# Optimization experiments

Measured on AMD Instinct MI355X. Metric: run time of the kernel, lower is better.

## Reference

```python
import jax, jax.numpy as jnp
import numpy as np
from jax import lax

N_LAYERS, N_HIDDEN, IN_DIM, WARMUP, T_STEPS = 3, 1024, 256, 64, 2048


def setup_inputs() -> dict:
    key = jax.random.key(0)
    ks = jax.random.split(key, 16)
    s = 0.03  # keep gate pre-activations sane
    return {
        "x": jax.random.uniform(ks[0], (1, IN_DIM, WARMUP), jnp.float32),
        "h0": jax.random.normal(ks[1], (N_LAYERS, N_HIDDEN), jnp.float32),
        "c0": jax.random.normal(ks[2], (N_LAYERS, N_HIDDEN), jnp.float32),
        "W_ih0": jax.random.normal(ks[3], (4 * N_HIDDEN, IN_DIM), jnp.float32) * s,
        "W_hh0": jax.random.normal(ks[4], (4 * N_HIDDEN, N_HIDDEN), jnp.float32) * s,
        "W_ih1": jax.random.normal(ks[5], (4 * N_HIDDEN, N_HIDDEN), jnp.float32) * s,
        "W_hh1": jax.random.normal(ks[6], (4 * N_HIDDEN, N_HIDDEN), jnp.float32) * s,
        "W_ih2": jax.random.normal(ks[7], (4 * N_HIDDEN, N_HIDDEN), jnp.float32) * s,
        "W_hh2": jax.random.normal(ks[8], (4 * N_HIDDEN, N_HIDDEN), jnp.float32) * s,
        "b_ih": jax.random.normal(ks[9], (N_LAYERS, 4 * N_HIDDEN), jnp.float32) * s,
        "b_hh": jax.random.normal(ks[10], (N_LAYERS, 4 * N_HIDDEN), jnp.float32) * s,
        "W_fc": jax.random.normal(ks[11], (IN_DIM, N_HIDDEN), jnp.float32) * s,
        "b_fc": jax.random.normal(ks[12], (IN_DIM,), jnp.float32) * s,
        "timesteps": T_STEPS,
    }


def _lstm_cell(inp, h, c, W_ih, W_hh, bi, bh):
    # PyTorch gate order: i, f, g, o
    g = W_ih @ inp + W_hh @ h + bi + bh  # (4H,)
    i, f, gg, o = jnp.split(g, 4)
    c_new = jax.nn.sigmoid(f) * c + jax.nn.sigmoid(i) * jnp.tanh(gg)
    h_new = jax.nn.sigmoid(o) * jnp.tanh(c_new)
    return h_new, c_new


def reference(x, h0, c0, W_ih0, W_hh0, W_ih1, W_hh1, W_ih2, W_hh2, b_ih, b_hh, W_fc, b_fc, timesteps):
    T = int(timesteps)
    L = x.shape[2]
    D = x.shape[1]
    x_seq = x[0].T  # (L, D) teacher-forcing inputs (batch must be 1, per original reshape)
    x_pad = jnp.zeros((T, D), x.dtype).at[:L].set(x_seq)

    def step(carry, s):
        h, c, prev = carry  # h, c: (3, H)
        h = lax.stop_gradient(h)  # hn.detach()
        c = lax.stop_gradient(c)  # cn.detach()
        inp = jnp.where(s < L, x_pad[s], prev)
        h0n, c0n = _lstm_cell(inp, h[0], c[0], W_ih0, W_hh0, b_ih[0], b_hh[0])
        h1n, c1n = _lstm_cell(h0n, h[1], c[1], W_ih1, W_hh1, b_ih[1], b_hh[1])
        h2n, c2n = _lstm_cell(h1n, h[2], c[2], W_ih2, W_hh2, b_ih[2], b_hh[2])
        gen = jax.nn.sigmoid(W_fc @ lax.stop_gradient(h2n) + b_fc)  # fc on detached lstm out
        nxt = jnp.where(s + 1 < L, x_pad[s + 1], gen)
        new_carry = (jnp.stack([h0n, h1n, h2n]), jnp.stack([c0n, c1n, c2n]), nxt)
        return new_carry, nxt

    init = (h0, c0, x_seq[0])
    _, outs = lax.scan(step, init, jnp.arange(T - 1))  # (T-1, D)
    out = jnp.concatenate([x_seq[0:1], outs], axis=0)  # (T, D)
    return out.T[None]  # (1, D, T)
```

## Files before the change

### kernel.cpp

```cpp
#include <hip/hip_runtime.h>
#include <math.h>

#define H 1024
#define D 256
#define NB 256
#define NT 512
#define LW 64
#define STRIDE 32

typedef float f32x4 __attribute__((ext_vector_type(4)));

__device__ __forceinline__ float sigf(float v) { return 1.f / (1.f + __expf(-v)); }

__device__ __forceinline__ float waveReduce(float v) {
#pragma unroll
    for (int off = 32; off > 0; off >>= 1) v += __shfl_xor(v, off, 64);
    return v;
}

__device__ __forceinline__ f32x4 ldg4_nw(const float* p) {
    f32x4 r;
    asm volatile("global_load_dwordx4 %0, %1, off sc0 sc1" : "=v"(r) : "v"(p) : "memory");
    return r;
}
__device__ __forceinline__ float ldg1_nw(const float* p) {
    float r;
    asm volatile("global_load_dword %0, %1, off sc0 sc1" : "=v"(r) : "v"(p) : "memory");
    return r;
}
__device__ __forceinline__ void vm_wait4(f32x4& a, f32x4& b, f32x4& c, f32x4& d) {
    asm volatile("s_waitcnt vmcnt(0)" : "+v"(a), "+v"(b), "+v"(c), "+v"(d) :: "memory");
    __builtin_amdgcn_sched_barrier(0);
}
__device__ __forceinline__ void vm_wait4f(float& a, float& b, float& c, float& d) {
    asm volatile("s_waitcnt vmcnt(0)" : "+v"(a), "+v"(b), "+v"(c), "+v"(d) :: "memory");
    __builtin_amdgcn_sched_barrier(0);
}
__device__ __forceinline__ void stg4_sc(float* p, f32x4 v) {
    asm volatile("global_store_dwordx4 %0, %1, off sc0 sc1" :: "v"(p), "v"(v) : "memory");
}
__device__ __forceinline__ void stg1_sc(float* p, float v) {
    asm volatile("global_store_dword %0, %1, off sc0 sc1" :: "v"(p), "v"(v) : "memory");
}

__device__ __forceinline__ float tagf(int i) { return 8.0f * (float)(i & 3) - 12.0f; }
__device__ __forceinline__ bool vld4(f32x4 c, float tg) {
    float m = fmaxf(fmaxf(fabsf(c.x - tg), fabsf(c.y - tg)),
                    fmaxf(fabsf(c.z - tg), fabsf(c.w - tg)));
    return m < 2.0f;
}

#define EXN ((1 + 6) * NB * STRIDE)
__device__ float g_ex[EXN];

__global__ void ws_clear() {
    int i = blockIdx.x * blockDim.x + threadIdx.x;
    for (; i < EXN; i += gridDim.x * blockDim.x) g_ex[i] = 0.f;
}

__global__ __launch_bounds__(NT, 2) void rnn_reg8(
    const float* __restrict__ x, const float* __restrict__ h0in, const float* __restrict__ c0,
    const float* __restrict__ Wih0, const float* __restrict__ Whh0,
    const float* __restrict__ Wih1, const float* __restrict__ Whh1,
    const float* __restrict__ Wih2, const float* __restrict__ Whh2,
    const float* __restrict__ b_ih, const float* __restrict__ b_hh,
    const float* __restrict__ Wfc, const float* __restrict__ bfc,
    float* __restrict__ out, int T, int L)
{
    const int b = blockIdx.x;
    const int tid = threadIdx.x;
    const int w = tid >> 6;
    const int lane = tid & 63;
    const int gate = w & 3;
    const int up = w >> 2;
    const int u0 = b * 4 + 2 * up;
    const int r0 = gate * H + u0;
    const int r1 = r0 + 1;
    const int off = lane * 4;

    float* inpw = g_ex;

    __shared__ __align__(16) float lds_h0[2 * H], lds_h1[2 * H], lds_h2[2 * H];
    __shared__ __align__(16) float lds_fc[H];
    __shared__ __align__(16) float lds_inp[D];
    __shared__ float lds_x[LW];
    __shared__ float gate_buf[16];
    __shared__ float red[8];
    __shared__ float c_st[12];

    float4 wA0[5], wB0[5], wA1[8], wB1[8], wA2[8], wB2[8];
    wA0[0] = *(const float4*)(Wih0 + (size_t)r0 * 256 + off);
    wB0[0] = *(const float4*)(Wih0 + (size_t)r1 * 256 + off);
#pragma unroll
    for (int j = 0; j < 4; ++j) {
        wA0[j + 1] = *(const float4*)(Whh0 + (size_t)r0 * H + j * 256 + off);
        wB0[j + 1] = *(const float4*)(Whh0 + (size_t)r1 * H + j * 256 + off);
        wA1[j]     = *(const float4*)(Wih1 + (size_t)r0 * H + j * 256 + off);
        wB1[j]     = *(const float4*)(Wih1 + (size_t)r1 * H + j * 256 + off);
        wA1[j + 4] = *(const float4*)(Whh1 + (size_t)r0 * H + j * 256 + off);
        wB1[j + 4] = *(const float4*)(Whh1 + (size_t)r1 * H + j * 256 + off);
        wA2[j]     = *(const float4*)(Wih2 + (size_t)r0 * H + j * 256 + off);
        wB2[j]     = *(const float4*)(Wih2 + (size_t)r1 * H + j * 256 + off);
        wA2[j + 4] = *(const float4*)(Whh2 + (size_t)r0 * H + j * 256 + off);
        wB2[j + 4] = *(const float4*)(Whh2 + (size_t)r1 * H + j * 256 + off);
    }
    const float bA0 = b_ih[r0] + b_hh[r0];
    const float bB0 = b_ih[r1] + b_hh[r1];
    const float bA1 = b_ih[4 * H + r0] + b_hh[4 * H + r0];
    const float bB1 = b_ih[4 * H + r1] + b_hh[4 * H + r1];
    const float bA2 = b_ih[8 * H + r0] + b_hh[8 * H + r0];
    const float bB2 = b_ih[8 * H + r1] + b_hh[8 * H + r1];
    const float bfc_b = bfc[b];

#define KA(v) asm volatile("" : "+v"(v.x), "+v"(v.y), "+v"(v.z), "+v"(v.w))
#pragma unroll
    for (int j = 0; j < 5; ++j) { KA(wA0[j]); KA(wB0[j]); }
#pragma unroll
    for (int j = 0; j < 8; ++j) { KA(wA1[j]); KA(wB1[j]); KA(wA2[j]); KA(wB2[j]); }
#undef KA

    for (int i = tid; i < H; i += NT) {
        lds_fc[i]     = Wfc[(size_t)b * H + i];
        lds_h0[H + i] = h0in[i];
        lds_h1[H + i] = h0in[H + i];
        lds_h2[H + i] = h0in[2 * H + i];
    }
    if (tid < LW && tid < L) lds_x[tid] = x[(size_t)b * L + tid];
    if (tid < 12) c_st[tid] = c0[(tid >> 2) * H + b * 4 + (tid & 3)];
    if (tid == 0) {
        float v = x[(size_t)b * L];
        out[(size_t)b * T] = v;
        stg1_sc(inpw + b * STRIDE, v + tagf(0));
    }
    __syncthreads();

#define POLLH(SRC, DST, TG)                                                    \
    if (w == 0) {                                                              \
        const float* s_ = (SRC); float* d_ = (DST); const float tg_ = (TG);    \
        bool d0 = false, d1 = false, d2 = false, d3 = false;                   \
        int spin = 0;                                                          \
        for (;;) {                                                             \
            f32x4 c0 = {0,0,0,0}, c1 = c0, c2 = c0, c3 = c0;                   \
            if (!d0) c0 = ldg4_nw(s_ + lane * STRIDE);                         \
            if (!d1) c1 = ldg4_nw(s_ + (lane + 64) * STRIDE);                  \
            if (!d2) c2 = ldg4_nw(s_ + (lane + 128) * STRIDE);                 \
            if (!d3) c3 = ldg4_nw(s_ + (lane + 192) * STRIDE);                 \
            vm_wait4(c0, c1, c2, c3);                                          \
            if (!d0 && vld4(c0, tg_)) { d0 = true;                             \
                f32x4 u = {c0.x-tg_, c0.y-tg_, c0.z-tg_, c0.w-tg_};            \
                *(f32x4*)(d_ + lane * 4) = u; }                                \
            if (!d1 && vld4(c1, tg_)) { d1 = true;                             \
                f32x4 u = {c1.x-tg_, c1.y-tg_, c1.z-tg_, c1.w-tg_};            \
                *(f32x4*)(d_ + (lane + 64) * 4) = u; }                         \
            if (!d2 && vld4(c2, tg_)) { d2 = true;                             \
                f32x4 u = {c2.x-tg_, c2.y-tg_, c2.z-tg_, c2.w-tg_};            \
                *(f32x4*)(d_ + (lane + 128) * 4) = u; }                        \
            if (!d3 && vld4(c3, tg_)) { d3 = true;                             \
                f32x4 u = {c3.x-tg_, c3.y-tg_, c3.z-tg_, c3.w-tg_};            \
                *(f32x4*)(d_ + (lane + 192) * 4) = u; }                        \
            if (__all(d0 && d1 && d2 && d3)) break;                            \
            if (++spin > 1) __builtin_amdgcn_s_sleep(8);                       \
        }                                                                      \
    }

#define DOT(WA, WB, N1, P1, N2, P2, BA, BB)                                   \
    {                                                                         \
        float4 a0 = {0,0,0,0}, a1 = {0,0,0,0};                                \
        _Pragma("unroll")                                                     \
        for (int j = 0; j < N1; ++j) {                                        \
            float4 v = *(const float4*)((P1) + j * 256 + off);                \
            a0.x += WA[j].x*v.x; a0.y += WA[j].y*v.y;                         \
            a0.z += WA[j].z*v.z; a0.w += WA[j].w*v.w;                         \
            a1.x += WB[j].x*v.x; a1.y += WB[j].y*v.y;                         \
            a1.z += WB[j].z*v.z; a1.w += WB[j].w*v.w;                         \
        }                                                                     \
        _Pragma("unroll")                                                     \
        for (int j = 0; j < N2; ++j) {                                        \
            float4 v = *(const float4*)((P2) + j * 256 + off);                \
            a0.x += WA[N1+j].x*v.x; a0.y += WA[N1+j].y*v.y;                   \
            a0.z += WA[N1+j].z*v.z; a0.w += WA[N1+j].w*v.w;                   \
            a1.x += WB[N1+j].x*v.x; a1.y += WB[N1+j].y*v.y;                   \
            a1.z += WB[N1+j].z*v.z; a1.w += WB[N1+j].w*v.w;                   \
        }                                                                     \
        float s0 = waveReduce(a0.x + a0.y + a0.z + a0.w);                     \
        float s1 = waveReduce(a1.x + a1.y + a1.z + a1.w);                     \
        if (lane == 0) {                                                      \
            gate_buf[(2*up)*4 + gate]   = s0 + BA;                            \
            gate_buf[(2*up+1)*4 + gate] = s1 + BB;                            \
        }                                                                     \
    }

#define COMBINE(LIDX, HGPTR, TG)                                              \
    if (w == 7) {                                                             \
        float hn = 0.f;                                                       \
        if (lane < 4) {                                                       \
            float gi = gate_buf[lane*4+0], gf = gate_buf[lane*4+1];           \
            float gg = gate_buf[lane*4+2], go = gate_buf[lane*4+3];           \
            float cn = sigf(gf)*c_st[(LIDX)*4+lane] + sigf(gi)*tanhf(gg);     \
            c_st[(LIDX)*4+lane] = cn;                                         \
            hn = sigf(go)*tanhf(cn);                                          \
        }                                                                     \
        float v0=__shfl(hn,0), v1=__shfl(hn,1), v2=__shfl(hn,2), v3=__shfl(hn,3); \
        if (lane == 0) {                                                      \
            f32x4 pk = {v0+(TG), v1+(TG), v2+(TG), v3+(TG)};                  \
            stg4_sc((HGPTR) + b*STRIDE, pk);                                  \
        }                                                                     \
    }

    for (int s = 0; s < T - 1; ++s) {
        const int ps = s & 1;
        const float tagS = tagf(s);
        float* hg0 = g_ex + (1 + 0 * 2 + ps) * NB * STRIDE;
        float* hg1 = g_ex + (1 + 1 * 2 + ps) * NB * STRIDE;
        float* hg2 = g_ex + (1 + 2 * 2 + ps) * NB * STRIDE;

        if (w == 0) {
            bool e0 = false, e1 = false, e2 = false, e3 = false;
            int spin = 0;
            for (;;) {
                float c0 = 0.f, c1 = 0.f, c2 = 0.f, c3 = 0.f;
                if (!e0) c0 = ldg1_nw(inpw + lane * STRIDE);
                if (!e1) c1 = ldg1_nw(inpw + (lane + 64) * STRIDE);
                if (!e2) c2 = ldg1_nw(inpw + (lane + 128) * STRIDE);
                if (!e3) c3 = ldg1_nw(inpw + (lane + 192) * STRIDE);
                vm_wait4f(c0, c1, c2, c3);
                if (!e0 && fabsf(c0 - tagS) < 2.f) { e0 = true; lds_inp[lane]       = c0 - tagS; }
                if (!e1 && fabsf(c1 - tagS) < 2.f) { e1 = true; lds_inp[lane + 64]  = c1 - tagS; }
                if (!e2 && fabsf(c2 - tagS) < 2.f) { e2 = true; lds_inp[lane + 128] = c2 - tagS; }
                if (!e3 && fabsf(c3 - tagS) < 2.f) { e3 = true; lds_inp[lane + 192] = c3 - tagS; }
                if (__all(e0 && e1 && e2 && e3)) break;
                if (++spin > 1) __builtin_amdgcn_s_sleep(8);
            }
        }
        __syncthreads();
        DOT(wA0, wB0, 1, lds_inp, 4, lds_h0 + (ps ^ 1) * H, bA0, bB0)
        __syncthreads();
        COMBINE(0, hg0, tagS)

        POLLH(hg0, lds_h0 + ps * H, tagS)
        __syncthreads();
        DOT(wA1, wB1, 4, lds_h0 + ps * H, 4, lds_h1 + (ps ^ 1) * H, bA1, bB1)
        __syncthreads();
        COMBINE(1, hg1, tagS)

        POLLH(hg1, lds_h1 + ps * H, tagS)
        __syncthreads();
        DOT(wA2, wB2, 4, lds_h1 + ps * H, 4, lds_h2 + (ps ^ 1) * H, bA2, bB2)
        __syncthreads();
        COMBINE(2, hg2, tagS)

        POLLH(hg2, lds_h2 + ps * H, tagS)
        __syncthreads();
        if (s + 1 >= L) {
            float2 pv = *(const float2*)(lds_h2 + ps * H + 2 * tid);
            float2 fw = *(const float2*)(lds_fc + 2 * tid);
            float a = waveReduce(pv.x * fw.x + pv.y * fw.y);
            if (lane == 0) red[w] = a;
            __syncthreads();
        }
        if (w == 7 && lane == 0) {
            float nxt;
            if (s + 1 < L) {
                nxt = lds_x[s + 1];
            } else {
                float sfc = red[0] + red[1] + red[2] + red[3]
                          + red[4] + red[5] + red[6] + red[7];
                nxt = sigf(sfc + bfc_b);
            }
            out[(size_t)b * T + s + 1] = nxt;
            stg1_sc(inpw + b * STRIDE, nxt + tagf(s + 1));
        }
    }
#undef DOT
#undef COMBINE
#undef POLLH
}

extern "C" void kernel_launch(void* const* d_in, const int* in_sizes, int n_in,
                              void* d_out, int out_size, void* d_ws, size_t ws_size,
                              hipStream_t stream) {
    const float* x    = (const float*)d_in[0];
    const float* h0   = (const float*)d_in[1];
    const float* c0   = (const float*)d_in[2];
    const float* Wih0 = (const float*)d_in[3];
    const float* Whh0 = (const float*)d_in[4];
    const float* Wih1 = (const float*)d_in[5];
    const float* Whh1 = (const float*)d_in[6];
    const float* Wih2 = (const float*)d_in[7];
    const float* Whh2 = (const float*)d_in[8];
    const float* bih  = (const float*)d_in[9];
    const float* bhh  = (const float*)d_in[10];
    const float* Wfc  = (const float*)d_in[11];
    const float* bfc  = (const float*)d_in[12];

    float* out = (float*)d_out;

    int T = out_size / D;
    int L = in_sizes[0] / D;

    ws_clear<<<64, 256, 0, stream>>>();

    void* args[] = { &x, &h0, &c0, &Wih0, &Whh0, &Wih1, &Whh1, &Wih2, &Whh2,
                     &bih, &bhh, &Wfc, &bfc, &out, &T, &L };

    (void)hipLaunchCooperativeKernel((void*)rnn_reg8, dim3(NB), dim3(NT), args, 0, stream);
}
```

Measured before the change: 24.45 ms.

## Pack inter-block exchange buffers densely and parallelize polling across four waves

Replaces the strided (32-float padded) cross-block exchange slots with a densely packed layout, so each block's published hidden values and input token sit contiguously. Polling for hidden-state chunks is spread across four waves, with one lane per producer block, instead of one wave issuing four loads per lane. Input-token polling now uses one vector load per lane. Each block also writes its own results straight into LDS and skips polling itself, and the sleep backoff is shortened. The aim is lower latency per synchronization round. The cost is more false sharing on cache lines and more waves spinning on polls.

```diff
diff --git a/kernel.cpp b/kernel.cpp
--- a/kernel.cpp
+++ b/kernel.cpp
@@ -6,7 +6,6 @@
 #define NB 256
 #define NT 512
 #define LW 64
-#define STRIDE 32
 
 typedef float f32x4 __attribute__((ext_vector_type(4)));
 
@@ -23,17 +22,8 @@
     asm volatile("global_load_dwordx4 %0, %1, off sc0 sc1" : "=v"(r) : "v"(p) : "memory");
     return r;
 }
-__device__ __forceinline__ float ldg1_nw(const float* p) {
-    float r;
-    asm volatile("global_load_dword %0, %1, off sc0 sc1" : "=v"(r) : "v"(p) : "memory");
-    return r;
-}
-__device__ __forceinline__ void vm_wait4(f32x4& a, f32x4& b, f32x4& c, f32x4& d) {
-    asm volatile("s_waitcnt vmcnt(0)" : "+v"(a), "+v"(b), "+v"(c), "+v"(d) :: "memory");
-    __builtin_amdgcn_sched_barrier(0);
-}
-__device__ __forceinline__ void vm_wait4f(float& a, float& b, float& c, float& d) {
-    asm volatile("s_waitcnt vmcnt(0)" : "+v"(a), "+v"(b), "+v"(c), "+v"(d) :: "memory");
+__device__ __forceinline__ void vm_wait1(f32x4& a) {
+    asm volatile("s_waitcnt vmcnt(0)" : "+v"(a) :: "memory");
     __builtin_amdgcn_sched_barrier(0);
 }
 __device__ __forceinline__ void stg4_sc(float* p, f32x4 v) {
@@ -50,7 +40,7 @@
     return m < 2.0f;
 }
 
-#define EXN ((1 + 6) * NB * STRIDE)
+#define EXN (256 + 6 * H)
 __device__ float g_ex[EXN];
 
 __global__ void ws_clear() {
@@ -58,7 +48,7 @@
     for (; i < EXN; i += gridDim.x * blockDim.x) g_ex[i] = 0.f;
 }
 
-__global__ __launch_bounds__(NT, 2) void rnn_reg8(
+__global__ __launch_bounds__(NT, 2) void rnn_reg9(
     const float* __restrict__ x, const float* __restrict__ h0in, const float* __restrict__ c0,
     const float* __restrict__ Wih0, const float* __restrict__ Whh0,
     const float* __restrict__ Wih1, const float* __restrict__ Whh1,
@@ -130,36 +120,31 @@
     if (tid == 0) {
         float v = x[(size_t)b * L];
         out[(size_t)b * T] = v;
-        stg1_sc(inpw + b * STRIDE, v + tagf(0));
+        lds_inp[b] = v;
+        stg1_sc(inpw + b, v + tagf(0));
     }
     __syncthreads();
 
 #define POLLH(SRC, DST, TG)                                                    \
-    if (w == 0) {                                                              \
-        const float* s_ = (SRC); float* d_ = (DST); const float tg_ = (TG);    \
-        bool d0 = false, d1 = false, d2 = false, d3 = false;                   \
+    if (w < 4) {                                                               \
+        const int c_ = w * 64 + lane;                                          \
+        const float* s_ = (SRC) + c_ * 4;                                      \
+        float* d_ = (DST) + c_ * 4;                                            \
+        const float tg_ = (TG);                                                \
+        bool done = (c_ == b);                                                 \
         int spin = 0;                                                          \
         for (;;) {                                                             \
-            f32x4 c0 = {0,0,0,0}, c1 = c0, c2 = c0, c3 = c0;                   \
-            if (!d0) c0 = ldg4_nw(s_ + lane * STRIDE);                         \
-            if (!d1) c1 = ldg4_nw(s_ + (lane + 64) * STRIDE);                  \
-            if (!d2) c2 = ldg4_nw(s_ + (lane + 128) * STRIDE);                 \
-            if (!d3) c3 = ldg4_nw(s_ + (lane + 192) * STRIDE);                 \
-            vm_wait4(c0, c1, c2, c3);                                          \
-            if (!d0 && vld4(c0, tg_)) { d0 = true;                             \
-                f32x4 u = {c0.x-tg_, c0.y-tg_, c0.z-tg_, c0.w-tg_};            \
-                *(f32x4*)(d_ + lane * 4) = u; }                                \
-            if (!d1 && vld4(c1, tg_)) { d1 = true;                             \
-                f32x4 u = {c1.x-tg_, c1.y-tg_, c1.z-tg_, c1.w-tg_};            \
-                *(f32x4*)(d_ + (lane + 64) * 4) = u; }                         \
-            if (!d2 && vld4(c2, tg_)) { d2 = true;                             \
-                f32x4 u = {c2.x-tg_, c2.y-tg_, c2.z-tg_, c2.w-tg_};            \
-                *(f32x4*)(d_ + (lane + 128) * 4) = u; }                        \
-            if (!d3 && vld4(c3, tg_)) { d3 = true;                             \
-                f32x4 u = {c3.x-tg_, c3.y-tg_, c3.z-tg_, c3.w-tg_};            \
-                *(f32x4*)(d_ + (lane + 192) * 4) = u; }                        \
-            if (__all(d0 && d1 && d2 && d3)) break;                            \
-            if (++spin > 1) __builtin_amdgcn_s_sleep(8);                       \
+            f32x4 v = {0, 0, 0, 0};                                            \
+            if (!done) v = ldg4_nw(s_);                                        \
+            vm_wait1(v);                                                       \
+            if (!done && vld4(v, tg_)) {                                       \
+                f32x4 u = {v.x - tg_, v.y - tg_, v.z - tg_, v.w - tg_};        \
+                *(f32x4*)d_ = u;                                               \
+                done = true;                                                   \
+            }                                                                  \
+            if (__all(done)) break;                                            \
+            if (++spin > 8) __builtin_amdgcn_s_sleep(4);                       \
+            else            __builtin_amdgcn_s_sleep(1);                       \
         }                                                                      \
     }
 
@@ -190,7 +175,7 @@
         }                                                                     \
     }
 
-#define COMBINE(LIDX, HGPTR, TG)                                              \
+#define COMBINE(LIDX, HGPTR, TG, MIRROR)                                      \
     if (w == 7) {                                                             \
         float hn = 0.f;                                                       \
         if (lane < 4) {                                                       \
@@ -203,51 +188,51 @@
         float v0=__shfl(hn,0), v1=__shfl(hn,1), v2=__shfl(hn,2), v3=__shfl(hn,3); \
         if (lane == 0) {                                                      \
             f32x4 pk = {v0+(TG), v1+(TG), v2+(TG), v3+(TG)};                  \
-            stg4_sc((HGPTR) + b*STRIDE, pk);                                  \
+            stg4_sc((HGPTR) + b*4, pk);                                       \
+            f32x4 raw = {v0, v1, v2, v3};                                     \
+            *(f32x4*)((MIRROR) + b*4) = raw;                                  \
         }                                                                     \
     }
 
     for (int s = 0; s < T - 1; ++s) {
         const int ps = s & 1;
         const float tagS = tagf(s);
-        float* hg0 = g_ex + (1 + 0 * 2 + ps) * NB * STRIDE;
-        float* hg1 = g_ex + (1 + 1 * 2 + ps) * NB * STRIDE;
-        float* hg2 = g_ex + (1 + 2 * 2 + ps) * NB * STRIDE;
+        float* hg0 = g_ex + 256 + (0 * 2 + ps) * H;
+        float* hg1 = g_ex + 256 + (1 * 2 + ps) * H;
+        float* hg2 = g_ex + 256 + (2 * 2 + ps) * H;
 
         if (w == 0) {
-            bool e0 = false, e1 = false, e2 = false, e3 = false;
+            const int e = lane * 4;
+            bool d0 = (e == b), d1 = (e + 1 == b), d2 = (e + 2 == b), d3 = (e + 3 == b);
             int spin = 0;
             for (;;) {
-                float c0 = 0.f, c1 = 0.f, c2 = 0.f, c3 = 0.f;
-                if (!e0) c0 = ldg1_nw(inpw + lane * STRIDE);
-                if (!e1) c1 = ldg1_nw(inpw + (lane + 64) * STRIDE);
-                if (!e2) c2 = ldg1_nw(inpw + (lane + 128) * STRIDE);
-                if (!e3) c3 = ldg1_nw(inpw + (lane + 192) * STRIDE);
-                vm_wait4f(c0, c1, c2, c3);
-                if (!e0 && fabsf(c0 - tagS) < 2.f) { e0 = true; lds_inp[lane]       = c0 - tagS; }
-                if (!e1 && fabsf(c1 - tagS) < 2.f) { e1 = true; lds_inp[lane + 64]  = c1 - tagS; }
-                if (!e2 && fabsf(c2 - tagS) < 2.f) { e2 = true; lds_inp[lane + 128] = c2 - tagS; }
-                if (!e3 && fabsf(c3 - tagS) < 2.f) { e3 = true; lds_inp[lane + 192] = c3 - tagS; }
-                if (__all(e0 && e1 && e2 && e3)) break;
-                if (++spin > 1) __builtin_amdgcn_s_sleep(8);
+                f32x4 v = ldg4_nw(inpw + e);
+                vm_wait1(v);
+                if (!d0 && fabsf(v.x - tagS) < 2.f) { d0 = true; lds_inp[e]     = v.x - tagS; }
+                if (!d1 && fabsf(v.y - tagS) < 2.f) { d1 = true; lds_inp[e + 1] = v.y - tagS; }
+                if (!d2 && fabsf(v.z - tagS) < 2.f) { d2 = true; lds_inp[e + 2] = v.z - tagS; }
+                if (!d3 && fabsf(v.w - tagS) < 2.f) { d3 = true; lds_inp[e + 3] = v.w - tagS; }
+                if (__all(d0 && d1 && d2 && d3)) break;
+                if (++spin > 8) __builtin_amdgcn_s_sleep(4);
+                else            __builtin_amdgcn_s_sleep(1);
             }
         }
         __syncthreads();
         DOT(wA0, wB0, 1, lds_inp, 4, lds_h0 + (ps ^ 1) * H, bA0, bB0)
         __syncthreads();
-        COMBINE(0, hg0, tagS)
+        COMBINE(0, hg0, tagS, lds_h0 + ps * H)
 
         POLLH(hg0, lds_h0 + ps * H, tagS)
         __syncthreads();
         DOT(wA1, wB1, 4, lds_h0 + ps * H, 4, lds_h1 + (ps ^ 1) * H, bA1, bB1)
         __syncthreads();
-        COMBINE(1, hg1, tagS)
+        COMBINE(1, hg1, tagS, lds_h1 + ps * H)
 
         POLLH(hg1, lds_h1 + ps * H, tagS)
         __syncthreads();
         DOT(wA2, wB2, 4, lds_h1 + ps * H, 4, lds_h2 + (ps ^ 1) * H, bA2, bB2)
         __syncthreads();
-        COMBINE(2, hg2, tagS)
+        COMBINE(2, hg2, tagS, lds_h2 + ps * H)
 
         POLLH(hg2, lds_h2 + ps * H, tagS)
         __syncthreads();
@@ -268,7 +253,8 @@
                 nxt = sigf(sfc + bfc_b);
             }
             out[(size_t)b * T + s + 1] = nxt;
-            stg1_sc(inpw + b * STRIDE, nxt + tagf(s + 1));
+            lds_inp[b] = nxt;
+            stg1_sc(inpw + b, nxt + tagf(s + 1));
         }
     }
 #undef DOT
@@ -298,10 +284,10 @@
     int T = out_size / D;
     int L = in_sizes[0] / D;
 
-    ws_clear<<<64, 256, 0, stream>>>();
+    ws_clear<<<16, 512, 0, stream>>>();
 
     void* args[] = { &x, &h0, &c0, &Wih0, &Whh0, &Wih1, &Whh1, &Wih2, &Whh2,
                      &bih, &bhh, &Wfc, &bfc, &out, &T, &L };
 
-    (void)hipLaunchCooperativeKernel((void*)rnn_reg8, dim3(NB), dim3(NT), args, 0, stream);
-}
+    (void)hipLaunchCooperativeKernel((void*)rnn_reg9, dim3(NB), dim3(NT), args, 0, stream);
+}
```

Measured after the change: 25.60 ms. 1.05x slower.
